# Kernel tuning notes

Hardware: AMD Instinct MI355X
Metric: run time of the kernel (lower is better)

Reference implementation:

```python
import jax, jax.numpy as jnp
import numpy as np

B, N, D = 16, 1024, 1024  # head_count = 1, N must equal D for shapes to close


def setup_inputs() -> dict:
    key = jax.random.key(0)
    kx, kk, kq, kv, kr = jax.random.split(key, 5)
    s = 1.0 / np.sqrt(D)  # keep pre-softmax logits in a sane range
    return {
        "x": jax.random.normal(kx, (B, N, D), dtype=jnp.float32),
        "Wk": jax.random.normal(kk, (D, D), dtype=jnp.float32) * s,
        "Wq": jax.random.normal(kq, (D, D), dtype=jnp.float32) * s,
        "Wv": jax.random.normal(kv, (D, D), dtype=jnp.float32) * s,
        "Wr": jax.random.normal(kr, (D, D), dtype=jnp.float32) * s,
    }


def reference(x, Wk, Wq, Wv, Wr):
    # torch nn.Linear(bias=False): y = x @ W.T
    keys = x @ Wk.T      # [B, N, D]
    queries = x @ Wq.T   # [B, N, D]
    values = x @ Wv.T    # [B, N, D]

    d = Wk.shape[0]  # head_key_channels = head_value_channels = D (head_count=1)
    # Faithful to the torch code: slice dim=1 (tokens) to the first D entries.
    # With N == D this is the full tensor.
    key = jax.nn.softmax(keys[:, :d, :], axis=2)      # softmax over channels
    query = jax.nn.softmax(queries[:, :d, :], axis=1)  # softmax over tokens
    value = values[:, :d, :]

    # context = key @ value^T : [B, d, d]
    context = jnp.einsum('bnd,bmd->bnm', key, value)
    # attended = context^T @ query : [B, d, D]
    attended = jnp.einsum('bnm,bnd->bmd', context, query)

    return attended @ Wr.T  # [B, d, D]
```

## Files before the change

kernel.cpp:

```cpp
#include <hip/hip_runtime.h>

typedef unsigned short u16;
typedef unsigned int u32;
typedef __attribute__((ext_vector_type(4))) float f32x4;
typedef __attribute__((ext_vector_type(8))) short bf16x8;
typedef __attribute__((ext_vector_type(4))) u16 u16x4;
typedef __attribute__((ext_vector_type(8))) u16 u16x8;

#define B_ 16
#define N_ 1024
#define D_ 1024
#define BM 256
#define BN 256
#define BK 64
#define TILE_BYTES (BM * BK * 2)

__device__ __forceinline__ float bf2f(u16 v) {
  return __uint_as_float((u32)v << 16);
}
__device__ __forceinline__ u16 f2bf(float f) {
  u32 u = __float_as_uint(f);
  return (u16)((u + 0x7FFFu + ((u >> 16) & 1u)) >> 16);
}
__device__ __forceinline__ void gload_lds16(const void* g, void* l) {
  __builtin_amdgcn_global_load_lds(
      (const __attribute__((address_space(1))) void*)g,
      (__attribute__((address_space(3))) void*)l, 16, 0, 0);
}

__global__ __launch_bounds__(256) void cast_kernel(const float* __restrict__ in,
                                                   u16* __restrict__ out, int n4) {
  const int stride = gridDim.x * blockDim.x;
  for (int i = blockIdx.x * blockDim.x + threadIdx.x; i < n4; i += stride) {
    float4 v = ((const float4*)in)[i];
    u16x4 o;
    o[0] = f2bf(v.x); o[1] = f2bf(v.y); o[2] = f2bf(v.z); o[3] = f2bf(v.w);
    ((u16x4*)out)[i] = o;
  }
}

__global__ __launch_bounds__(256) void cast4_kernel(
    const float* __restrict__ w0, const float* __restrict__ w1,
    const float* __restrict__ w2, const float* __restrict__ w3,
    u16* __restrict__ out) {
  const int per = (D_ * D_) / 4;
  const int stride = gridDim.x * blockDim.x;
  for (int i = blockIdx.x * blockDim.x + threadIdx.x; i < 4 * per; i += stride) {
    const int w = i / per, r = i - w * per;
    const float* src = (w == 0) ? w0 : (w == 1) ? w1 : (w == 2) ? w2 : w3;
    float4 v = ((const float4*)src)[r];
    u16x4 o;
    o[0] = f2bf(v.x); o[1] = f2bf(v.y); o[2] = f2bf(v.z); o[3] = f2bf(v.w);
    ((u16x4*)out)[i] = o;
  }
}

template <typename OutT>
__global__ __launch_bounds__(512, 2) void gemm_bt256(
    const u16* __restrict__ A, const u16* __restrict__ Bm, OutT* __restrict__ C,
    int K, int ldc, long long sA, long long sB, long long sC,
    int tx_n, int nb_per) {
  __shared__ u16 lds[2][2][BM * BK];
  const int tid = threadIdx.x;
  const int lane = tid & 63;
  const int wid = tid >> 6;
  const int wm = wid >> 2;
  const int wn = wid & 3;
  const int rl = lane & 15, kl = lane >> 4;

  const int orig = blockIdx.x;
  const int wgid = ((orig & 7) << 5) | (orig >> 3);
  const int batch = wgid / nb_per;
  const int rem = wgid % nb_per;
  const int row0 = (rem / tx_n) * BM, col0 = (rem % tx_n) * BN;
  A += (long long)batch * sA;
  Bm += (long long)batch * sB;
  C += (long long)batch * sC;

  auto ldsTile = [&](int buf, int ab) -> char* {
    return (char*)&lds[0][0][0] + (size_t)(buf * 2 + ab) * TILE_BYTES;
  };

  auto stageA = [&](int t, int buf) {
    char* base = ldsTile(buf, 0);
#pragma unroll
    for (int g = 0; g < 4; ++g) {
      const int d = g * 8192 + tid * 16;
      const int r = d >> 7;
      const int li = (d & 127) ^ ((r & 7) << 4);
      gload_lds16(A + (size_t)(row0 + r) * K + t * BK + (li >> 1), base + d);
    }
  };
  auto stageB = [&](int t, int buf) {
    char* base = ldsTile(buf, 1);
#pragma unroll
    for (int g = 0; g < 4; ++g) {
      const int d = g * 8192 + tid * 16;
      const int r = d >> 7;
      const int li = (d & 127) ^ ((r & 7) << 4);
      gload_lds16(Bm + (size_t)(col0 + r) * K + t * BK + (li >> 1), base + d);
    }
  };
  auto rdA = [&](int buf, int mi, int kk) -> bf16x8 {
    const int R = wm * 128 + mi * 16 + rl;
    const int p = (R * 128 + kk * 64 + kl * 16) ^ ((R & 7) << 4);
    return *(const bf16x8*)(ldsTile(buf, 0) + p);
  };
  auto rdB = [&](int buf, int ni, int kk) -> bf16x8 {
    const int R = wn * 64 + ni * 16 + rl;
    const int p = (R * 128 + kk * 64 + kl * 16) ^ ((R & 7) << 4);
    return *(const bf16x8*)(ldsTile(buf, 1) + p);
  };

  f32x4 acc[8][4] = {};
  bf16x8 aF[4][2], bF[4][2];

  stageB(0, 0); stageA(0, 0);
  stageB(1, 1); stageA(1, 1);
  asm volatile("s_waitcnt vmcnt(8)" ::: "memory");
  __builtin_amdgcn_s_barrier();

  const int nt = K / BK;
  for (int t = 0; t < nt; ++t) {
    const int cur = t & 1;
    const bool pf = (t + 2) < nt;
#pragma unroll
    for (int mi = 0; mi < 4; ++mi) {
      aF[mi][0] = rdA(cur, mi, 0); aF[mi][1] = rdA(cur, mi, 1);
    }
#pragma unroll
    for (int ni = 0; ni < 4; ++ni) {
      bF[ni][0] = rdB(cur, ni, 0); bF[ni][1] = rdB(cur, ni, 1);
    }
#pragma unroll
    for (int kk = 0; kk < 2; ++kk)
#pragma unroll
      for (int mi = 0; mi < 4; ++mi)
#pragma unroll
        for (int ni = 0; ni < 4; ++ni)
          acc[mi][ni] = __builtin_amdgcn_mfma_f32_16x16x32_bf16(
              aF[mi][kk], bF[ni][kk], acc[mi][ni], 0, 0, 0);
    __builtin_amdgcn_sched_barrier(0);
    __builtin_amdgcn_s_barrier();
    if (pf) stageB(t + 2, cur);
#pragma unroll
    for (int mi = 0; mi < 4; ++mi) {
      aF[mi][0] = rdA(cur, 4 + mi, 0); aF[mi][1] = rdA(cur, 4 + mi, 1);
    }
#pragma unroll
    for (int kk = 0; kk < 2; ++kk)
#pragma unroll
      for (int mi = 0; mi < 4; ++mi)
#pragma unroll
        for (int ni = 0; ni < 4; ++ni)
          acc[4 + mi][ni] = __builtin_amdgcn_mfma_f32_16x16x32_bf16(
              aF[mi][kk], bF[ni][kk], acc[4 + mi][ni], 0, 0, 0);
    __builtin_amdgcn_sched_barrier(0);
    if (pf) asm volatile("s_waitcnt vmcnt(4)" ::: "memory");
    else    asm volatile("s_waitcnt vmcnt(0)" ::: "memory");
    __builtin_amdgcn_s_barrier();
    if (pf) stageA(t + 2, cur);
  }
#pragma unroll
  for (int mi = 0; mi < 8; ++mi)
#pragma unroll
    for (int ni = 0; ni < 4; ++ni)
#pragma unroll
      for (int j = 0; j < 4; ++j) {
        const int rr = row0 + wm * 128 + mi * 16 + kl * 4 + j;
        const int cc = col0 + wn * 64 + ni * 16 + rl;
        const float v = acc[mi][ni][j];
        if constexpr (sizeof(OutT) == 2)
          C[(size_t)rr * ldc + cc] = (OutT)f2bf(v);
        else
          C[(size_t)rr * ldc + cc] = v;
      }
}

__global__ __launch_bounds__(256) void key_sm_t(const u16* __restrict__ Kp,
                                                u16* __restrict__ KT) {
  const int b = blockIdx.y, n0 = blockIdx.x * 64;
  const int tid = threadIdx.x, lane = tid & 63, w = tid >> 6;
  __shared__ float smax[64], sinv[64];
  __shared__ u16 Tl[64][72];
  const u16* base = Kp + ((size_t)b * N_ + n0) * D_;
  for (int i = 0; i < 16; ++i) {
    const int r = w * 16 + i;
    const u16x8* rp = (const u16x8*)(base + (size_t)r * D_ + lane * 16);
    u16x8 v0 = rp[0], v1 = rp[1];
    float f[16];
#pragma unroll
    for (int j = 0; j < 8; ++j) { f[j] = bf2f(v0[j]); f[8 + j] = bf2f(v1[j]); }
    float m = -1e30f;
#pragma unroll
    for (int j = 0; j < 16; ++j) m = fmaxf(m, f[j]);
    for (int off = 32; off; off >>= 1) m = fmaxf(m, __shfl_xor(m, off));
    float s = 0.f;
#pragma unroll
    for (int j = 0; j < 16; ++j) s += __expf(f[j] - m);
    for (int off = 32; off; off >>= 1) s += __shfl_xor(s, off);
    if (lane == 0) { smax[r] = m; sinv[r] = 1.f / s; }
  }
  __syncthreads();
  for (int ct = 0; ct < 16; ++ct) {
    const int r = tid >> 2, cb = (tid & 3) * 16;
    const u16x8* rp = (const u16x8*)(base + (size_t)r * D_ + ct * 64 + cb);
    u16x8 v0 = rp[0], v1 = rp[1];
    const float m = smax[r], inv = sinv[r];
#pragma unroll
    for (int j = 0; j < 8; ++j) {
      Tl[r][cb + j] = f2bf(__expf(bf2f(v0[j]) - m) * inv);
      Tl[r][cb + 8 + j] = f2bf(__expf(bf2f(v1[j]) - m) * inv);
    }
    __syncthreads();
    const int c = tid >> 2, nb = (tid & 3) * 16;
    u16x8 o0, o1;
#pragma unroll
    for (int e = 0; e < 8; ++e) { o0[e] = Tl[nb + e][c]; o1[e] = Tl[nb + 8 + e][c]; }
    u16x8* op = (u16x8*)(KT + ((size_t)b * D_ + ct * 64 + c) * N_ + n0 + nb);
    op[0] = o0; op[1] = o1;
    __syncthreads();
  }
}

__global__ __launch_bounds__(256) void query_sm_t(const u16* __restrict__ Qp,
                                                  u16* __restrict__ QT) {
  const int b = blockIdx.y, d0 = blockIdx.x * 64;
  const int tid = threadIdx.x, l = tid & 63, g = tid >> 6;
  __shared__ float pm[4][64], ps[4][64];
  __shared__ float cmax[64], cinv[64];
  __shared__ u16 Tl[64][72];
  const u16* base = Qp + (size_t)b * N_ * D_;
  float m = -1e30f, s = 0.f;
  for (int n = g * 256; n < g * 256 + 256; ++n) {
    const float x = bf2f(base[(size_t)n * D_ + d0 + l]);
    const float nm = fmaxf(m, x);
    s = s * __expf(m - nm) + __expf(x - nm);
    m = nm;
  }
  pm[g][l] = m; ps[g][l] = s;
  __syncthreads();
  if (tid < 64) {
    float M = pm[0][tid];
    for (int k2 = 1; k2 < 4; ++k2) M = fmaxf(M, pm[k2][tid]);
    float S = 0.f;
    for (int k2 = 0; k2 < 4; ++k2) S += ps[k2][tid] * __expf(pm[k2][tid] - M);
    cmax[tid] = M; cinv[tid] = 1.f / S;
  }
  __syncthreads();
  for (int nt = 0; nt < 16; ++nt) {
    const int r = tid >> 2, cb = (tid & 3) * 16;
    const u16x8* rp = (const u16x8*)(base + (size_t)(nt * 64 + r) * D_ + d0 + cb);
    u16x8 v0 = rp[0], v1 = rp[1];
#pragma unroll
    for (int j = 0; j < 8; ++j) {
      Tl[r][cb + j] = f2bf(__expf(bf2f(v0[j]) - cmax[cb + j]) * cinv[cb + j]);
      Tl[r][cb + 8 + j] =
          f2bf(__expf(bf2f(v1[j]) - cmax[cb + 8 + j]) * cinv[cb + 8 + j]);
    }
    __syncthreads();
    const int c = tid >> 2, nb = (tid & 3) * 16;
    u16x8 o0, o1;
#pragma unroll
    for (int e = 0; e < 8; ++e) { o0[e] = Tl[nb + e][c]; o1[e] = Tl[nb + 8 + e][c]; }
    u16x8* op = (u16x8*)(QT + ((size_t)b * D_ + d0 + c) * N_ + nt * 64 + nb);
    op[0] = o0; op[1] = o1;
    __syncthreads();
  }
}

extern "C" void kernel_launch(void* const* d_in, const int* in_sizes, int n_in,
                              void* d_out, int out_size, void* d_ws, size_t ws_size,
                              hipStream_t stream) {
  const float* x = (const float*)d_in[0];
  const float* Wk = (const float*)d_in[1];
  const float* Wq = (const float*)d_in[2];
  const float* Wv = (const float*)d_in[3];
  const float* Wr = (const float*)d_in[4];
  float* out = (float*)d_out;
  char* ws = (char*)d_ws;
  const size_t MB = 1ull << 20;

  u16* Xb  = (u16*)(ws + 0 * MB);
  u16* KT  = (u16*)(ws + 0 * MB);
  u16* Wkb = (u16*)(ws + 32 * MB);
  u16* Wqb = (u16*)(ws + 34 * MB);
  u16* Wvb = (u16*)(ws + 36 * MB);
  u16* Wrb = (u16*)(ws + 38 * MB);
  u16* Kp  = (u16*)(ws + 40 * MB);
  u16* St  = (u16*)(ws + 40 * MB);
  u16* Qp  = (u16*)(ws + 72 * MB);
  u16* Att = (u16*)(ws + 72 * MB);
  u16* V   = (u16*)(ws + 104 * MB);
  u16* QT  = (u16*)(ws + 136 * MB);

  const int nX = B_ * N_ * D_;
  cast_kernel<<<2048, 256, 0, stream>>>(x, Xb, nX / 4);
  cast4_kernel<<<1024, 256, 0, stream>>>(Wk, Wq, Wv, Wr, Wkb);

  gemm_bt256<u16><<<256, 512, 0, stream>>>(Xb, Wkb, Kp, D_, D_, 0, 0, 0, 4, 256);
  gemm_bt256<u16><<<256, 512, 0, stream>>>(Xb, Wqb, Qp, D_, D_, 0, 0, 0, 4, 256);
  gemm_bt256<u16><<<256, 512, 0, stream>>>(Xb, Wvb, V, D_, D_, 0, 0, 0, 4, 256);

  key_sm_t<<<dim3(N_ / 64, B_), 256, 0, stream>>>(Kp, KT);
  query_sm_t<<<dim3(D_ / 64, B_), 256, 0, stream>>>(Qp, QT);

  const long long sNN = (long long)N_ * D_;
  gemm_bt256<u16><<<256, 512, 0, stream>>>(QT, KT, St, N_, D_, sNN, sNN, sNN, 4, 16);
  gemm_bt256<u16><<<256, 512, 0, stream>>>(V, St, Att, D_, D_, sNN, sNN, sNN, 4, 16);
  gemm_bt256<float><<<256, 512, 0, stream>>>(Att, Wrb, out, D_, D_, 0, 0, 0, 4, 256);
}
```

Before: 309.2 us.

## Split GEMM K-loop into four quadrant phases with half-tile prefetch and setprio

Restructures the bf16 GEMM main loop into four 128x128 quadrant MFMA phases. Each phase is interleaved with a half-tile global-to-LDS load, so A for the next stage and B two stages ahead are streamed in 128-row regions. It adds s_setprio around MFMA clusters and explicit lgkmcnt waits so that LDS reads, global loads and matrix math overlap more finely. The cost is more barriers per iteration and more complex wait-count reasoning, which could cause stalls or races if the counts are wrong.

Measured after the change: 319.7 us. 3.4% more time.

```diff
diff --git a/kernel.cpp b/kernel.cpp
--- a/kernel.cpp
+++ b/kernel.cpp
@@ -13,7 +13,7 @@
 #define BM 256
 #define BN 256
 #define BK 64
-#define TILE_BYTES (BM * BK * 2)
+#define REGION_BYTES (128 * BK * 2)
 
 __device__ __forceinline__ float bf2f(u16 v) {
   return __uint_as_float((u32)v << 16);
@@ -60,7 +60,7 @@
     const u16* __restrict__ A, const u16* __restrict__ Bm, OutT* __restrict__ C,
     int K, int ldc, long long sA, long long sB, long long sC,
     int tx_n, int nb_per) {
-  __shared__ u16 lds[2][2][BM * BK];
+  __shared__ u16 lds[2][4][128 * BK];
   const int tid = threadIdx.x;
   const int lane = tid & 63;
   const int wid = tid >> 6;
@@ -77,89 +77,129 @@
   Bm += (long long)batch * sB;
   C += (long long)batch * sC;
 
-  auto ldsTile = [&](int buf, int ab) -> char* {
-    return (char*)&lds[0][0][0] + (size_t)(buf * 2 + ab) * TILE_BYTES;
+  auto region = [&](int buf, int rg) -> char* {
+    return (char*)&lds[0][0][0] + (size_t)(buf * 4 + rg) * REGION_BYTES;
   };
 
-  auto stageA = [&](int t, int buf) {
-    char* base = ldsTile(buf, 0);
-#pragma unroll
-    for (int g = 0; g < 4; ++g) {
+  auto stageHalf = [&](const u16* src, int t, int buf, int rg, int grow0) {
+    char* base = region(buf, rg);
+#pragma unroll
+    for (int g = 0; g < 2; ++g) {
       const int d = g * 8192 + tid * 16;
       const int r = d >> 7;
       const int li = (d & 127) ^ ((r & 7) << 4);
-      gload_lds16(A + (size_t)(row0 + r) * K + t * BK + (li >> 1), base + d);
-    }
-  };
-  auto stageB = [&](int t, int buf) {
-    char* base = ldsTile(buf, 1);
-#pragma unroll
-    for (int g = 0; g < 4; ++g) {
-      const int d = g * 8192 + tid * 16;
-      const int r = d >> 7;
-      const int li = (d & 127) ^ ((r & 7) << 4);
-      gload_lds16(Bm + (size_t)(col0 + r) * K + t * BK + (li >> 1), base + d);
+      gload_lds16(src + (size_t)(grow0 + r) * K + t * BK + (li >> 1), base + d);
     }
   };
   auto rdA = [&](int buf, int mi, int kk) -> bf16x8 {
     const int R = wm * 128 + mi * 16 + rl;
-    const int p = (R * 128 + kk * 64 + kl * 16) ^ ((R & 7) << 4);
-    return *(const bf16x8*)(ldsTile(buf, 0) + p);
+    const int r = R & 127;
+    const int p = (r * 128 + kk * 64 + kl * 16) ^ ((r & 7) << 4);
+    return *(const bf16x8*)(region(buf, R >> 7) + p);
   };
   auto rdB = [&](int buf, int ni, int kk) -> bf16x8 {
-    const int R = wn * 64 + ni * 16 + rl;
-    const int p = (R * 128 + kk * 64 + kl * 16) ^ ((R & 7) << 4);
-    return *(const bf16x8*)(ldsTile(buf, 1) + p);
+    const int Rb = wn * 64 + ni * 16 + rl;
+    const int r = Rb & 127;
+    const int p = (r * 128 + kk * 64 + kl * 16) ^ ((r & 7) << 4);
+    return *(const bf16x8*)(region(buf, 2 + (Rb >> 7)) + p);
   };
 
   f32x4 acc[8][4] = {};
-  bf16x8 aF[4][2], bF[4][2];
-
-  stageB(0, 0); stageA(0, 0);
-  stageB(1, 1); stageA(1, 1);
-  asm volatile("s_waitcnt vmcnt(8)" ::: "memory");
+  bf16x8 aF[4][2], bF[2][2], bG[2][2];
+
+  stageHalf(A, 0, 0, 0, row0);  stageHalf(A, 0, 0, 1, row0 + 128);
+  stageHalf(Bm, 0, 0, 2, col0); stageHalf(Bm, 0, 0, 3, col0 + 128);
+  stageHalf(Bm, 1, 1, 2, col0); stageHalf(Bm, 1, 1, 3, col0 + 128);
+  asm volatile("s_waitcnt vmcnt(4)" ::: "memory");
   __builtin_amdgcn_s_barrier();
 
   const int nt = K / BK;
   for (int t = 0; t < nt; ++t) {
     const int cur = t & 1;
-    const bool pf = (t + 2) < nt;
 #pragma unroll
     for (int mi = 0; mi < 4; ++mi) {
       aF[mi][0] = rdA(cur, mi, 0); aF[mi][1] = rdA(cur, mi, 1);
     }
 #pragma unroll
-    for (int ni = 0; ni < 4; ++ni) {
+    for (int ni = 0; ni < 2; ++ni) {
       bF[ni][0] = rdB(cur, ni, 0); bF[ni][1] = rdB(cur, ni, 1);
     }
+    if (t + 1 < nt) stageHalf(A, t + 1, cur ^ 1, 0, row0);
+    asm volatile("s_waitcnt lgkmcnt(8)" ::: "memory");
+    __builtin_amdgcn_sched_barrier(0);
+    __builtin_amdgcn_s_barrier();
+    asm volatile("s_waitcnt lgkmcnt(0)" ::: "memory");
+    __builtin_amdgcn_sched_barrier(0);
+    __builtin_amdgcn_s_setprio(1);
 #pragma unroll
     for (int kk = 0; kk < 2; ++kk)
 #pragma unroll
       for (int mi = 0; mi < 4; ++mi)
 #pragma unroll
-        for (int ni = 0; ni < 4; ++ni)
+        for (int ni = 0; ni < 2; ++ni)
           acc[mi][ni] = __builtin_amdgcn_mfma_f32_16x16x32_bf16(
               aF[mi][kk], bF[ni][kk], acc[mi][ni], 0, 0, 0);
-    __builtin_amdgcn_sched_barrier(0);
-    __builtin_amdgcn_s_barrier();
-    if (pf) stageB(t + 2, cur);
+    __builtin_amdgcn_s_setprio(0);
+    __builtin_amdgcn_sched_barrier(0);
+    __builtin_amdgcn_s_barrier();
+#pragma unroll
+    for (int ni = 0; ni < 2; ++ni) {
+      bG[ni][0] = rdB(cur, 2 + ni, 0); bG[ni][1] = rdB(cur, 2 + ni, 1);
+    }
+    if (t + 1 < nt) stageHalf(A, t + 1, cur ^ 1, 1, row0 + 128);
+    __builtin_amdgcn_sched_barrier(0);
+    __builtin_amdgcn_s_barrier();
+    asm volatile("s_waitcnt lgkmcnt(0)" ::: "memory");
+    __builtin_amdgcn_sched_barrier(0);
+    __builtin_amdgcn_s_setprio(1);
+#pragma unroll
+    for (int kk = 0; kk < 2; ++kk)
+#pragma unroll
+      for (int mi = 0; mi < 4; ++mi)
+#pragma unroll
+        for (int ni = 0; ni < 2; ++ni)
+          acc[mi][2 + ni] = __builtin_amdgcn_mfma_f32_16x16x32_bf16(
+              aF[mi][kk], bG[ni][kk], acc[mi][2 + ni], 0, 0, 0);
+    __builtin_amdgcn_s_setprio(0);
+    __builtin_amdgcn_sched_barrier(0);
+    __builtin_amdgcn_s_barrier();
 #pragma unroll
     for (int mi = 0; mi < 4; ++mi) {
       aF[mi][0] = rdA(cur, 4 + mi, 0); aF[mi][1] = rdA(cur, 4 + mi, 1);
     }
+    if (t + 2 < nt) stageHalf(Bm, t + 2, cur, 2, col0);
+    __builtin_amdgcn_sched_barrier(0);
+    __builtin_amdgcn_s_barrier();
+    asm volatile("s_waitcnt lgkmcnt(0)" ::: "memory");
+    __builtin_amdgcn_sched_barrier(0);
+    __builtin_amdgcn_s_setprio(1);
 #pragma unroll
     for (int kk = 0; kk < 2; ++kk)
 #pragma unroll
       for (int mi = 0; mi < 4; ++mi)
 #pragma unroll
-        for (int ni = 0; ni < 4; ++ni)
+        for (int ni = 0; ni < 2; ++ni)
+          acc[4 + mi][2 + ni] = __builtin_amdgcn_mfma_f32_16x16x32_bf16(
+              aF[mi][kk], bG[ni][kk], acc[4 + mi][2 + ni], 0, 0, 0);
+    __builtin_amdgcn_s_setprio(0);
+    __builtin_amdgcn_sched_barrier(0);
+    __builtin_amdgcn_s_barrier();
+    if (t + 2 < nt) stageHalf(Bm, t + 2, cur, 3, col0 + 128);
+    __builtin_amdgcn_sched_barrier(0);
+    __builtin_amdgcn_s_setprio(1);
+#pragma unroll
+    for (int kk = 0; kk < 2; ++kk)
+#pragma unroll
+      for (int mi = 0; mi < 4; ++mi)
+#pragma unroll
+        for (int ni = 0; ni < 2; ++ni)
           acc[4 + mi][ni] = __builtin_amdgcn_mfma_f32_16x16x32_bf16(
               aF[mi][kk], bF[ni][kk], acc[4 + mi][ni], 0, 0, 0);
-    __builtin_amdgcn_sched_barrier(0);
-    if (pf) asm volatile("s_waitcnt vmcnt(4)" ::: "memory");
-    else    asm volatile("s_waitcnt vmcnt(0)" ::: "memory");
-    __builtin_amdgcn_s_barrier();
-    if (pf) stageA(t + 2, cur);
+    __builtin_amdgcn_s_setprio(0);
+    __builtin_amdgcn_sched_barrier(0);
+    if (t + 2 < nt)      asm volatile("s_waitcnt vmcnt(4)" ::: "memory");
+    else if (t + 1 < nt) asm volatile("s_waitcnt vmcnt(0)" ::: "memory");
+    if (t + 1 < nt) __builtin_amdgcn_s_barrier();
   }
 #pragma unroll
   for (int mi = 0; mi < 8; ++mi)
```
